# Performance work log

Hardware: AMD Instinct MI355X
Metric: run time of the kernel (lower is better)

Reference implementation:

```python
import jax, jax.numpy as jnp
import numpy as np

C = 256      # channels
G = 8        # groups
K = 9        # 3x3 sampling points (DCNv4 default kernel_size=3)
DWK = 3      # dw_kernel_size (wrapper passes kernel_size=3)
OFFSET_SCALE = 1.0
N, H, W = 8, 64, 64


def setup_inputs() -> dict:
    key = jax.random.key(0)
    ks = jax.random.split(key, 6)
    def init(k, shape, fan):
        return jax.random.normal(k, shape, jnp.float32) * (fan ** -0.5)
    return {
        "x": jax.random.normal(ks[0], (N, C, H, W), jnp.float32),
        "dw_w": init(ks[1], (C, 1, DWK, DWK), DWK * DWK),   # depthwise conv (OIHW, groups=C)
        "dw_b": jnp.zeros((C,), jnp.float32),
        "om_w": init(ks[2], (G * K * 3, C), C) * 0.01,       # offset/mask linear (small offsets)
        "om_b": jnp.zeros((G * K * 3,), jnp.float32),
        "vp_w": init(ks[3], (C, C), C),                      # value_proj
        "vp_b": jnp.zeros((C,), jnp.float32),
        "op_w": init(ks[4], (C, C), C),                      # output_proj (output_bias=False)
    }


def reference(x, dw_w, dw_b, om_w, om_b, vp_w, vp_b, op_w):
    n, c, h, w = x.shape
    cg = c // G
    L = h * w
    # b c h w -> b (h w) c
    xf = x.transpose(0, 2, 3, 1).reshape(n, L, c)
    value = (xf @ vp_w.T + vp_b).reshape(n, L, G, cg)
    # offset/mask branch: depthwise conv on raw input, then linear
    om_in = jax.lax.conv_general_dilated(
        x, dw_w, (1, 1), "SAME", feature_group_count=c,
        dimension_numbers=("NCHW", "OIHW", "NCHW")) + dw_b[None, :, None, None]
    om = om_in.transpose(0, 2, 3, 1).reshape(n, L, c) @ om_w.T + om_b  # (n, L, G*K*3)
    om = om.reshape(n, h, w, G, K * 3)
    off = om[..., : 2 * K].reshape(n, h, w, G, K, 2) * OFFSET_SCALE     # (dy, dx) per point
    mask = om[..., 2 * K:]                                              # (n,h,w,G,K) raw (DCNv4: no softmax)
    # base 3x3 dilation-1 grid centered at each pixel
    d = jnp.arange(-1, 2, dtype=jnp.float32)
    dy, dx = jnp.meshgrid(d, d, indexing="ij")
    base = jnp.stack([dy.ravel(), dx.ravel()], -1)  # (K, 2)
    py = (jnp.arange(h, dtype=jnp.float32).reshape(1, h, 1, 1, 1)
          + base[:, 0].reshape(1, 1, 1, 1, K) + off[..., 0])  # (n,h,w,G,K)
    px = (jnp.arange(w, dtype=jnp.float32).reshape(1, 1, w, 1, 1)
          + base[:, 1].reshape(1, 1, 1, 1, K) + off[..., 1])
    y0 = jnp.floor(py); x0 = jnp.floor(px)
    ty = py - y0; tx = px - x0
    y0i = y0.astype(jnp.int32); x0i = x0.astype(jnp.int32)

    def gather(yi, xi, wgt):
        valid = (yi >= 0) & (yi < h) & (xi >= 0) & (xi < w)
        idx = jnp.clip(yi, 0, h - 1) * w + jnp.clip(xi, 0, w - 1)       # (n,h,w,G,K)
        idx = idx.transpose(0, 1, 2, 4, 3).reshape(n, L * K, G)[..., None]
        g = jnp.take_along_axis(value, idx, axis=1)                     # (n, L*K, G, cg)
        g = g.reshape(n, h, w, K, G, cg).transpose(0, 1, 2, 4, 3, 5)    # (n,h,w,G,K,cg)
        return g * (wgt * valid)[..., None]

    sampled = (gather(y0i,     x0i,     (1 - ty) * (1 - tx))
             + gather(y0i,     x0i + 1, (1 - ty) * tx)
             + gather(y0i + 1, x0i,     ty * (1 - tx))
             + gather(y0i + 1, x0i + 1, ty * tx))
    out = jnp.einsum("nhwgk,nhwgkc->nhwgc", mask, sampled)  # mask-weighted aggregation
    out = out.reshape(n, L, c) @ op_w.T                      # output_proj (no bias)
    # b (h w) c -> b c h w
    return out.reshape(n, h, w, c).transpose(0, 3, 1, 2)
```

## Files before the change

kernel.cpp:

```cpp
#include <hip/hip_runtime.h>
#include <hip/hip_fp16.h>
#include <math.h>

#define N_  8
#define C_  256
#define G_  8
#define CG_ 32
#define K_  9
#define H_  64
#define W_  64
#define L_  (H_*W_)
#define OM_ 216
#define OMP_ 256

using frag_ab = __attribute__((ext_vector_type(8))) short;
using frag_cd = __attribute__((ext_vector_type(4))) float;

__device__ __forceinline__ unsigned short f2bf(float f) {
    unsigned int u = __float_as_uint(f);
    u += 0x7FFFu + ((u >> 16) & 1u);
    return (unsigned short)(u >> 16);
}
__device__ __forceinline__ unsigned short f2h(float f) {
    return __half_as_ushort(__float2half(f));
}

__device__ __forceinline__ void gld16(const void* g, void* l) {
    __builtin_amdgcn_global_load_lds((const __attribute__((address_space(1))) void*)g,
                                     (__attribute__((address_space(3))) void*)l, 16, 0, 0);
}

__device__ __forceinline__ void tapcalc(int l, int k, float offy, float offx, float mk,
                                        float4& wq, uint4& sq) {
    const int y = l >> 6, xp = l & 63;
    float py = (float)(y + k / 3 - 1) + offy;
    float px = (float)(xp + k % 3 - 1) + offx;
    float fy = floorf(py), fx = floorf(px);
    float ty = py - fy, tx = px - fx;
    int y0 = (int)fy, x0i = (int)fx;
    int y1 = y0 + 1, x1 = x0i + 1;
    float vy0 = ((unsigned)y0 < (unsigned)H_) ? 1.f : 0.f;
    float vy1 = ((unsigned)y1 < (unsigned)H_) ? 1.f : 0.f;
    float vx0 = ((unsigned)x0i < (unsigned)W_) ? 1.f : 0.f;
    float vx1 = ((unsigned)x1 < (unsigned)W_) ? 1.f : 0.f;
    int cy0 = min(max(y0, 0), H_ - 1), cy1 = min(max(y1, 0), H_ - 1);
    int cx0 = min(max(x0i, 0), W_ - 1), cx1 = min(max(x1, 0), W_ - 1);
    wq = make_float4(mk * (1.f - ty) * (1.f - tx) * vy0 * vx0,
                     mk * (1.f - ty) * tx         * vy0 * vx1,
                     mk * ty         * (1.f - tx) * vy1 * vx0,
                     mk * ty         * tx         * vy1 * vx1);
    sq = make_uint4((unsigned)((cy0 * W_ + cx0) << 9),
                    (unsigned)((cy0 * W_ + cx1) << 9),
                    (unsigned)((cy1 * W_ + cx0) << 9),
                    (unsigned)((cy1 * W_ + cx1) << 9));
}

__global__ __launch_bounds__(256) void prep_kernel(const float* __restrict__ x,
                                                   const float* __restrict__ w,
                                                   const float* __restrict__ b,
                                                   const float* __restrict__ vp_w,
                                                   const float* __restrict__ om_w,
                                                   const float* __restrict__ om_b,
                                                   const float* __restrict__ op_w,
                                                   unsigned short* __restrict__ xb,
                                                   unsigned short* __restrict__ omb,
                                                   unsigned short* __restrict__ vp_wb,
                                                   unsigned short* __restrict__ om_wb,
                                                   float* __restrict__ om_bp,
                                                   unsigned short* __restrict__ op_wb) {
    const int n = blockIdx.z, y0 = blockIdx.y * 4, c0 = blockIdx.x * 32;
    const int tid = threadIdx.x;
    __shared__ float xs[6][32][66];
    __shared__ __align__(16) unsigned short os[2][64][40];
    for (int i = tid; i < 384; i += 256) {
        int r = i / 64, c = (i / 2) % 32, e = i & 1;
        xs[r][c][e * 65] = 0.f;
    }
    const float* xbase = x + ((size_t)n * C_ + c0) * L_;
    for (int i = tid; i < 6 * 32 * 16; i += 256) {
        int r = i >> 9, rem = i & 511, c = rem >> 4, x4 = (rem & 15) * 4;
        int yy = y0 + r - 1;
        float4 v = make_float4(0.f, 0.f, 0.f, 0.f);
        if ((unsigned)yy < (unsigned)H_) v = *(const float4*)(xbase + (size_t)c * L_ + yy * W_ + x4);
        xs[r][c][1 + x4] = v.x; xs[r][c][2 + x4] = v.y;
        xs[r][c][3 + x4] = v.z; xs[r][c][4 + x4] = v.w;
    }
    __syncthreads();

    const int c = tid & 31, x0 = (tid >> 5) * 8;
    float wv[9];
#pragma unroll
    for (int i = 0; i < 9; i++) wv[i] = w[(c0 + c) * 9 + i];
    const float bias = b[c0 + c];
    const int l = tid >> 2, c8 = (tid & 3) * 8;

    for (int rr = 0; rr < 4; rr++) {
        float o[8];
#pragma unroll
        for (int j = 0; j < 8; j++) o[j] = bias;
#pragma unroll
        for (int r = 0; r < 3; r++) {
            float v[10];
#pragma unroll
            for (int d = 0; d < 10; d++) v[d] = xs[rr + r][c][x0 + d];
#pragma unroll
            for (int j = 0; j < 8; j++)
                o[j] += wv[r * 3] * v[j] + wv[r * 3 + 1] * v[j + 1] + wv[r * 3 + 2] * v[j + 2];
        }
#pragma unroll
        for (int j = 0; j < 8; j++) {
            os[0][x0 + j][c] = f2bf(xs[rr + 1][c][1 + x0 + j]);
            os[1][x0 + j][c] = f2bf(o[j]);
        }
        __syncthreads();
        uint4 va = *(const uint4*)&os[0][l][c8];
        uint4 vc = *(const uint4*)&os[1][l][c8];
        size_t dst = (((size_t)n * 8 + blockIdx.x) * L_ + (y0 + rr) * W_ + l) * 32 + c8;
        *(uint4*)(xb + dst) = va;
        *(uint4*)(omb + dst) = vc;
        __syncthreads();
    }

    if (n == 0) {
        int base = (blockIdx.x + 8 * blockIdx.y) * 256 + tid;
#pragma unroll
        for (int rep2 = 0; rep2 < 2; rep2++) {
            int idx = base + rep2 * 32768;
            vp_wb[idx] = f2bf(vp_w[idx]);
            op_wb[idx] = f2bf(op_w[idx]);
            om_wb[idx] = (idx < OM_ * C_) ? f2bf(om_w[idx]) : (unsigned short)0;
        }
        if (base < OMP_) om_bp[base] = (base < OM_) ? om_b[base] : 0.f;
    }
}

__global__ __launch_bounds__(256, 2) void gemm12_kernel(const unsigned short* __restrict__ xb,
                                                        const unsigned short* __restrict__ omb,
                                                        const unsigned short* __restrict__ vp_wb,
                                                        const unsigned short* __restrict__ om_wb,
                                                        const float* __restrict__ vp_b,
                                                        const float* __restrict__ om_bp,
                                                        unsigned short* __restrict__ valueb,
                                                        float* __restrict__ omf) {
    __shared__ unsigned short As[128 * 32];
    __shared__ unsigned short Bs[256 * 32];
    const int which = blockIdx.z;
    const unsigned short* A = which ? omb : xb;
    const unsigned short* B = which ? om_wb : vp_wb;
    const float* bias = which ? om_bp : vp_b;
    const int tid = threadIdx.x;
    const long i0 = (long)blockIdx.x * 128;
    const int nA = (int)(i0 >> 12);
    const int lofs = (int)(i0 & 4095);
    const int wave = tid >> 6, lane = tid & 63;
    const int iw = (wave & 1) * 64, jw = (wave >> 1) * 128;
    const int lm = lane & 15, kq = lane >> 4;
    const int srow = tid >> 2, scol = (tid & 3) * 8;

    frag_cd acc[4][8];
#pragma unroll
    for (int a = 0; a < 4; a++)
#pragma unroll
        for (int c = 0; c < 8; c++) acc[a][c] = (frag_cd){0.f, 0.f, 0.f, 0.f};

    for (int k0 = 0; k0 < C_; k0 += 32) {
        const unsigned short* ga0 = A + (((size_t)nA * 8 + (k0 >> 5)) * L_ + lofs + srow) * 32 + scol;
        const unsigned short* gb0 = B + (long)srow * C_ + k0 + scol;
        gld16(ga0,             As + tid * 8);
        gld16(ga0 + 64 * 32,   As + 2048 + tid * 8);
        gld16(gb0,             Bs + tid * 8);
        gld16(gb0 + 64 * C_,   Bs + 2048 + tid * 8);
        gld16(gb0 + 128 * C_,  Bs + 4096 + tid * 8);
        gld16(gb0 + 192 * C_,  Bs + 6144 + tid * 8);
        __syncthreads();
        frag_ab af[4], bfr[8];
#pragma unroll
        for (int mi = 0; mi < 4; mi++)
            af[mi] = *(const frag_ab*)&As[(iw + mi * 16 + lm) * 32 + kq * 8];
#pragma unroll
        for (int ni = 0; ni < 8; ni++)
            bfr[ni] = *(const frag_ab*)&Bs[(jw + ni * 16 + lm) * 32 + kq * 8];
#pragma unroll
        for (int mi = 0; mi < 4; mi++)
#pragma unroll
            for (int ni = 0; ni < 8; ni++)
                acc[mi][ni] = __builtin_amdgcn_mfma_f32_16x16x32_bf16(af[mi], bfr[ni], acc[mi][ni], 0, 0, 0);
        __syncthreads();
    }

    float bv[8];
#pragma unroll
    for (int ni = 0; ni < 8; ni++)
        bv[ni] = bias[jw + ni * 16 + lm];

    const long ibase = i0 + iw + kq * 4;
    const int jbase = jw + lm;
#pragma unroll
    for (int mi = 0; mi < 4; mi++) {
#pragma unroll
        for (int ni = 0; ni < 8; ni++) {
            int jj = jbase + ni * 16;
#pragma unroll
            for (int r = 0; r < 4; r++) {
                long i = ibase + mi * 16 + r;
                float v = acc[mi][ni][r] + bv[ni];
                if (which)
                    omf[i * OMP_ + jj] = v;
                else
                    valueb[i * C_ + jj] = f2h(v);
            }
        }
    }
}

__global__ __launch_bounds__(256, 2) void samplegemm_kernel(const unsigned short* __restrict__ value,
                                                            const float* __restrict__ om,
                                                            const unsigned short* __restrict__ opw,
                                                            float* __restrict__ out) {
    const int n = blockIdx.x, l0 = blockIdx.y * 64;
    const int tid = threadIdx.x;
    __shared__ __align__(16) unsigned short interm[64 * 256];
    __shared__ __align__(16) float ombuf[8][224];
    __shared__ float4 wgt[64][9];
    __shared__ uint4  soff[64][9];

    const int wave = tid >> 6, lane = tid & 63;
    const int lp = tid >> 2;
    const int g = lp & 7;
    const int c8i = tid & 3;
    const int slot = tid & 31;
    const char* vbase = (const char*)(value + (size_t)n * L_ * C_);
    const char* vb = vbase + (size_t)(g * CG_ + c8i * 8) * 2;

    const float* omn = om + (size_t)n * L_ * OMP_;
    float* obase = &ombuf[2 * wave][0];

    const int s0row = (lane < 56) ? 0 : 1;
    const int s0idx = (lane < 56) ? lane : (lane - 56);

#define STAGE_OM(REP) { \
        const float* r0_ = omn + (size_t)(l0 + (REP) * 8 + 2 * wave) * OMP_; \
        gld16(r0_ + (size_t)s0row * OMP_ + s0idx * 4, obase); \
        if (lane < 48) gld16(r0_ + OMP_ + (8 + lane) * 4, (char*)obase + 1024); }

    STAGE_OM(0)

    for (int rep = 0; rep < 8; rep++) {
        asm volatile("s_waitcnt vmcnt(0)" ::: "memory");
#pragma unroll
        for (int j = 0; j < 3; j++) {
            if (!(j == 2 && lane >= 16)) {
                int it = lane + j * 64;
                int pl_loc = it / 9, k = it - pl_loc * 9;
                int pl = wave * 16 + pl_loc;
                int pic = pl >> 3;
                const float* ob2 = &ombuf[pic][(pl & 7) * 27];
                float offy = ob2[2 * k], offx = ob2[2 * k + 1], mk = ob2[18 + k];
                float4 wq; uint4 sq;
                tapcalc(l0 + rep * 8 + pic, k, offy, offx, mk, wq, sq);
                wgt[pl][k] = wq; soff[pl][k] = sq;
            }
        }
        asm volatile("" ::: "memory");
        if (rep < 7) STAGE_OM(rep + 1)
        asm volatile("" ::: "memory");
        const int p = rep * 8 + (lp >> 3);
        float acc[8] = {0.f, 0.f, 0.f, 0.f, 0.f, 0.f, 0.f, 0.f};
#pragma unroll
        for (int k = 0; k < K_; k++) {
            float4 wk = wgt[lp][k];
            uint4  ok = soff[lp][k];
            const uint4 v00 = *(const uint4*)(vb + ok.x);
            const uint4 v01 = *(const uint4*)(vb + ok.y);
            const uint4 v10 = *(const uint4*)(vb + ok.z);
            const uint4 v11 = *(const uint4*)(vb + ok.w);
#define ACC8(V, WW) { \
            const __half2* h_ = (const __half2*)&V; \
            acc[0] += WW * __half2float(h_[0].x); acc[1] += WW * __half2float(h_[0].y); \
            acc[2] += WW * __half2float(h_[1].x); acc[3] += WW * __half2float(h_[1].y); \
            acc[4] += WW * __half2float(h_[2].x); acc[5] += WW * __half2float(h_[2].y); \
            acc[6] += WW * __half2float(h_[3].x); acc[7] += WW * __half2float(h_[3].y); }
            ACC8(v00, wk.x) ACC8(v01, wk.y) ACC8(v10, wk.z) ACC8(v11, wk.w)
#undef ACC8
        }
        uint4 pk;
        unsigned short* ps = (unsigned short*)&pk;
#pragma unroll
        for (int i = 0; i < 8; i++) ps[i] = f2bf(acc[i]);
        int phys = slot ^ (p & 7);
        *(uint4*)&interm[p * 256 + phys * 8] = pk;
    }
#undef STAGE_OM
    __syncthreads();

    const int lm = lane & 15, kq = lane >> 4;
    const int q0w = wave * 64;
    frag_cd acc2[4][4];
#pragma unroll
    for (int a = 0; a < 4; a++)
#pragma unroll
        for (int c = 0; c < 4; c++) acc2[a][c] = (frag_cd){0.f, 0.f, 0.f, 0.f};

    for (int k0 = 0; k0 < C_; k0 += 32) {
        frag_ab af[4], bfr[4];
#pragma unroll
        for (int mi = 0; mi < 4; mi++)
            af[mi] = *(const frag_ab*)(opw + (size_t)(q0w + mi * 16 + lm) * C_ + k0 + kq * 8);
#pragma unroll
        for (int ni = 0; ni < 4; ni++) {
            int pxr = ni * 16 + lm;
            int phys = (k0 / 8 + kq) ^ (pxr & 7);
            bfr[ni] = *(const frag_ab*)&interm[pxr * 256 + phys * 8];
        }
#pragma unroll
        for (int mi = 0; mi < 4; mi++)
#pragma unroll
            for (int ni = 0; ni < 4; ni++)
                acc2[mi][ni] = __builtin_amdgcn_mfma_f32_16x16x32_bf16(af[mi], bfr[ni], acc2[mi][ni], 0, 0, 0);
    }

    float* ob = out + (size_t)n * C_ * L_ + l0;
#pragma unroll
    for (int mi = 0; mi < 4; mi++) {
#pragma unroll
        for (int ni = 0; ni < 4; ni++) {
            int pxr = ni * 16 + lm;
#pragma unroll
            for (int r = 0; r < 4; r++) {
                int q = q0w + mi * 16 + kq * 4 + r;
                ob[(size_t)q * L_ + pxr] = acc2[mi][ni][r];
            }
        }
    }
}

extern "C" void kernel_launch(void* const* d_in, const int* in_sizes, int n_in,
                              void* d_out, int out_size, void* d_ws, size_t ws_size,
                              hipStream_t stream) {
    const float* x    = (const float*)d_in[0];
    const float* dw_w = (const float*)d_in[1];
    const float* dw_b = (const float*)d_in[2];
    const float* om_w = (const float*)d_in[3];
    const float* om_b = (const float*)d_in[4];
    const float* vp_w = (const float*)d_in[5];
    const float* vp_b = (const float*)d_in[6];
    const float* op_w = (const float*)d_in[7];
    float* out = (float*)d_out;

    char* ws = (char*)d_ws;
    unsigned short* xb      = (unsigned short*)(ws);
    unsigned short* omb     = (unsigned short*)(ws + 16777216);
    unsigned short* valueb  = (unsigned short*)(ws + 33554432);
    float*          omf     = (float*)(ws + 50331648);
    unsigned short* vp_wb   = (unsigned short*)(ws + 83886080);
    unsigned short* om_wb   = (unsigned short*)(ws + 84017152);
    unsigned short* op_wb   = (unsigned short*)(ws + 84148224);
    float*          om_bp   = (float*)(ws + 84279296);

    prep_kernel<<<dim3(C_ / 32, H_ / 4, N_), 256, 0, stream>>>(
        x, dw_w, dw_b, vp_w, om_w, om_b, op_w,
        xb, omb, vp_wb, om_wb, om_bp, op_wb);
    gemm12_kernel<<<dim3(256, 1, 2), 256, 0, stream>>>(
        xb, omb, vp_wb, om_wb, vp_b, om_bp, valueb, omf);
    samplegemm_kernel<<<dim3(N_, L_ / 64), 256, 0, stream>>>(valueb, omf, op_wb, out);
}
```

Before: 166.8 us.

## Fuse three stages into one cooperative persistent kernel with grid syncs

Merges the prep, gemm12 and samplegemm kernels into a single cooperative launch of 512 blocks, separated by grid-wide syncs, with shared memory reused across stages. Each block handles two prep tiles, one GEMM tile and one sample tile. The aim is to remove kernel launch gaps and tail effects between the three stages. In exchange it adds the cost of grid barriers, and with a 60 KB shared buffer the block count may limit occupancy. It falls back to three separate launches if the cooperative launch fails.

```diff
diff --git a/kernel.cpp b/kernel.cpp
--- a/kernel.cpp
+++ b/kernel.cpp
@@ -1,6 +1,9 @@
 #include <hip/hip_runtime.h>
 #include <hip/hip_fp16.h>
+#include <hip/hip_cooperative_groups.h>
 #include <math.h>
+
+namespace cg = cooperative_groups;
 
 #define N_  8
 #define C_  256
@@ -55,23 +58,19 @@
                     (unsigned)((cy1 * W_ + cx1) << 9));
 }
 
-__global__ __launch_bounds__(256) void prep_kernel(const float* __restrict__ x,
-                                                   const float* __restrict__ w,
-                                                   const float* __restrict__ b,
-                                                   const float* __restrict__ vp_w,
-                                                   const float* __restrict__ om_w,
-                                                   const float* __restrict__ om_b,
-                                                   const float* __restrict__ op_w,
-                                                   unsigned short* __restrict__ xb,
-                                                   unsigned short* __restrict__ omb,
-                                                   unsigned short* __restrict__ vp_wb,
-                                                   unsigned short* __restrict__ om_wb,
-                                                   float* __restrict__ om_bp,
-                                                   unsigned short* __restrict__ op_wb) {
-    const int n = blockIdx.z, y0 = blockIdx.y * 4, c0 = blockIdx.x * 32;
-    const int tid = threadIdx.x;
-    __shared__ float xs[6][32][66];
-    __shared__ __align__(16) unsigned short os[2][64][40];
+
+__device__ __forceinline__ void prep_body(
+    int u, int tid,
+    const float* __restrict__ x, const float* __restrict__ w, const float* __restrict__ b,
+    const float* __restrict__ vp_w, const float* __restrict__ om_w,
+    const float* __restrict__ om_b, const float* __restrict__ op_w,
+    unsigned short* __restrict__ xb, unsigned short* __restrict__ omb,
+    unsigned short* __restrict__ vp_wb, unsigned short* __restrict__ om_wb,
+    float* __restrict__ om_bp, unsigned short* __restrict__ op_wb,
+    float (*xs)[32][66], unsigned short (*os)[64][40])
+{
+    const int bx = u & 7, by = (u >> 3) & 15, n = u >> 7;
+    const int y0 = by * 4, c0 = bx * 32;
     for (int i = tid; i < 384; i += 256) {
         int r = i / 64, c = (i / 2) % 32, e = i & 1;
         xs[r][c][e * 65] = 0.f;
@@ -115,14 +114,14 @@
         __syncthreads();
         uint4 va = *(const uint4*)&os[0][l][c8];
         uint4 vc = *(const uint4*)&os[1][l][c8];
-        size_t dst = (((size_t)n * 8 + blockIdx.x) * L_ + (y0 + rr) * W_ + l) * 32 + c8;
+        size_t dst = (((size_t)n * 8 + bx) * L_ + (y0 + rr) * W_ + l) * 32 + c8;
         *(uint4*)(xb + dst) = va;
         *(uint4*)(omb + dst) = vc;
         __syncthreads();
     }
 
     if (n == 0) {
-        int base = (blockIdx.x + 8 * blockIdx.y) * 256 + tid;
+        int base = (bx + 8 * by) * 256 + tid;
 #pragma unroll
         for (int rep2 = 0; rep2 < 2; rep2++) {
             int idx = base + rep2 * 32768;
@@ -134,22 +133,18 @@
     }
 }
 
-__global__ __launch_bounds__(256, 2) void gemm12_kernel(const unsigned short* __restrict__ xb,
-                                                        const unsigned short* __restrict__ omb,
-                                                        const unsigned short* __restrict__ vp_wb,
-                                                        const unsigned short* __restrict__ om_wb,
-                                                        const float* __restrict__ vp_b,
-                                                        const float* __restrict__ om_bp,
-                                                        unsigned short* __restrict__ valueb,
-                                                        float* __restrict__ omf) {
-    __shared__ unsigned short As[128 * 32];
-    __shared__ unsigned short Bs[256 * 32];
-    const int which = blockIdx.z;
+__device__ __forceinline__ void gemm12_body(
+    int bx, int which, int tid,
+    const unsigned short* __restrict__ xb, const unsigned short* __restrict__ omb,
+    const unsigned short* __restrict__ vp_wb, const unsigned short* __restrict__ om_wb,
+    const float* __restrict__ vp_b, const float* __restrict__ om_bp,
+    unsigned short* __restrict__ valueb, float* __restrict__ omf,
+    unsigned short* As, unsigned short* Bs)
+{
     const unsigned short* A = which ? omb : xb;
     const unsigned short* B = which ? om_wb : vp_wb;
     const float* bias = which ? om_bp : vp_b;
-    const int tid = threadIdx.x;
-    const long i0 = (long)blockIdx.x * 128;
+    const long i0 = (long)bx * 128;
     const int nA = (int)(i0 >> 12);
     const int lofs = (int)(i0 & 4095);
     const int wave = tid >> 6, lane = tid & 63;
@@ -213,17 +208,12 @@
     }
 }
 
-__global__ __launch_bounds__(256, 2) void samplegemm_kernel(const unsigned short* __restrict__ value,
-                                                            const float* __restrict__ om,
-                                                            const unsigned short* __restrict__ opw,
-                                                            float* __restrict__ out) {
-    const int n = blockIdx.x, l0 = blockIdx.y * 64;
-    const int tid = threadIdx.x;
-    __shared__ __align__(16) unsigned short interm[64 * 256];
-    __shared__ __align__(16) float ombuf[8][224];
-    __shared__ float4 wgt[64][9];
-    __shared__ uint4  soff[64][9];
-
+__device__ __forceinline__ void samplegemm_body(
+    int n, int l0, int tid,
+    const unsigned short* __restrict__ value, const float* __restrict__ om,
+    const unsigned short* __restrict__ opw, float* __restrict__ out,
+    unsigned short* interm, float (*ombuf)[224], float4 (*wgt)[9], uint4 (*soff)[9])
+{
     const int wave = tid >> 6, lane = tid & 63;
     const int lp = tid >> 2;
     const int g = lp & 7;
@@ -334,6 +324,91 @@
     }
 }
 
+__global__ __launch_bounds__(256, 2) void fused_kernel(
+    const float* __restrict__ x, const float* __restrict__ dw_w, const float* __restrict__ dw_b,
+    const float* __restrict__ om_w, const float* __restrict__ om_b,
+    const float* __restrict__ vp_w, const float* __restrict__ vp_b,
+    const float* __restrict__ op_w,
+    unsigned short* __restrict__ xb, unsigned short* __restrict__ omb,
+    unsigned short* __restrict__ valueb, float* __restrict__ omf,
+    unsigned short* __restrict__ vp_wb, unsigned short* __restrict__ om_wb,
+    unsigned short* __restrict__ op_wb, float* __restrict__ om_bp,
+    float* __restrict__ out)
+{
+    __shared__ __align__(16) char smem[60928];
+    const int bid = blockIdx.x;
+    const int tid = threadIdx.x;
+    cg::grid_group grid = cg::this_grid();
+
+    {
+        float (*xs)[32][66] = (float(*)[32][66])smem;
+        unsigned short (*os)[64][40] = (unsigned short(*)[64][40])(smem + 50688);
+        prep_body(bid * 2,     tid, x, dw_w, dw_b, vp_w, om_w, om_b, op_w,
+                  xb, omb, vp_wb, om_wb, om_bp, op_wb, xs, os);
+        prep_body(bid * 2 + 1, tid, x, dw_w, dw_b, vp_w, om_w, om_b, op_w,
+                  xb, omb, vp_wb, om_wb, om_bp, op_wb, xs, os);
+    }
+    __threadfence();
+    grid.sync();
+
+    {
+        unsigned short* As = (unsigned short*)smem;
+        unsigned short* Bs = (unsigned short*)(smem + 8192);
+        gemm12_body(bid & 255, bid >> 8, tid, xb, omb, vp_wb, om_wb,
+                    vp_b, om_bp, valueb, omf, As, Bs);
+    }
+    __threadfence();
+    grid.sync();
+
+    {
+        unsigned short* interm = (unsigned short*)smem;
+        float (*ombuf)[224] = (float(*)[224])(smem + 32768);
+        float4 (*wgt)[9]    = (float4(*)[9])(smem + 39936);
+        uint4 (*soff)[9]    = (uint4(*)[9])(smem + 49152);
+        samplegemm_body(bid & 7, (bid >> 3) * 64, tid, valueb, omf, op_wb, out,
+                        interm, ombuf, wgt, soff);
+    }
+}
+
+__global__ __launch_bounds__(256) void prep_kernel(
+    const float* __restrict__ x, const float* __restrict__ w, const float* __restrict__ b,
+    const float* __restrict__ vp_w, const float* __restrict__ om_w,
+    const float* __restrict__ om_b, const float* __restrict__ op_w,
+    unsigned short* __restrict__ xb, unsigned short* __restrict__ omb,
+    unsigned short* __restrict__ vp_wb, unsigned short* __restrict__ om_wb,
+    float* __restrict__ om_bp, unsigned short* __restrict__ op_wb)
+{
+    __shared__ float xs[6][32][66];
+    __shared__ __align__(16) unsigned short os[2][64][40];
+    int u = blockIdx.x + 8 * blockIdx.y + 128 * blockIdx.z;
+    prep_body(u, threadIdx.x, x, w, b, vp_w, om_w, om_b, op_w,
+              xb, omb, vp_wb, om_wb, om_bp, op_wb, xs, os);
+}
+
+__global__ __launch_bounds__(256, 2) void gemm12_kernel(
+    const unsigned short* __restrict__ xb, const unsigned short* __restrict__ omb,
+    const unsigned short* __restrict__ vp_wb, const unsigned short* __restrict__ om_wb,
+    const float* __restrict__ vp_b, const float* __restrict__ om_bp,
+    unsigned short* __restrict__ valueb, float* __restrict__ omf)
+{
+    __shared__ unsigned short As[128 * 32];
+    __shared__ unsigned short Bs[256 * 32];
+    gemm12_body(blockIdx.x, blockIdx.z, threadIdx.x, xb, omb, vp_wb, om_wb,
+                vp_b, om_bp, valueb, omf, As, Bs);
+}
+
+__global__ __launch_bounds__(256, 2) void samplegemm_kernel(
+    const unsigned short* __restrict__ value, const float* __restrict__ om,
+    const unsigned short* __restrict__ opw, float* __restrict__ out)
+{
+    __shared__ __align__(16) unsigned short interm[64 * 256];
+    __shared__ __align__(16) float ombuf[8][224];
+    __shared__ float4 wgt[64][9];
+    __shared__ uint4  soff[64][9];
+    samplegemm_body(blockIdx.x, blockIdx.y * 64, threadIdx.x, value, om, opw, out,
+                    interm, ombuf, wgt, soff);
+}
+
 extern "C" void kernel_launch(void* const* d_in, const int* in_sizes, int n_in,
                               void* d_out, int out_size, void* d_ws, size_t ws_size,
                               hipStream_t stream) {
@@ -357,10 +432,21 @@
     unsigned short* op_wb   = (unsigned short*)(ws + 84148224);
     float*          om_bp   = (float*)(ws + 84279296);
 
-    prep_kernel<<<dim3(C_ / 32, H_ / 4, N_), 256, 0, stream>>>(
-        x, dw_w, dw_b, vp_w, om_w, om_b, op_w,
-        xb, omb, vp_wb, om_wb, om_bp, op_wb);
-    gemm12_kernel<<<dim3(256, 1, 2), 256, 0, stream>>>(
-        xb, omb, vp_wb, om_wb, vp_b, om_bp, valueb, omf);
-    samplegemm_kernel<<<dim3(N_, L_ / 64), 256, 0, stream>>>(valueb, omf, op_wb, out);
-}
+    void* args[] = {
+        (void*)&x, (void*)&dw_w, (void*)&dw_b, (void*)&om_w, (void*)&om_b,
+        (void*)&vp_w, (void*)&vp_b, (void*)&op_w,
+        (void*)&xb, (void*)&omb, (void*)&valueb, (void*)&omf,
+        (void*)&vp_wb, (void*)&om_wb, (void*)&op_wb, (void*)&om_bp,
+        (void*)&out
+    };
+    hipError_t err = hipLaunchCooperativeKernel((void*)fused_kernel,
+                                                dim3(512), dim3(256), args, 0, stream);
+    if (err != hipSuccess) {
+        prep_kernel<<<dim3(C_ / 32, H_ / 4, N_), 256, 0, stream>>>(
+            x, dw_w, dw_b, vp_w, om_w, om_b, op_w,
+            xb, omb, vp_wb, om_wb, om_bp, op_wb);
+        gemm12_kernel<<<dim3(256, 1, 2), 256, 0, stream>>>(
+            xb, omb, vp_wb, om_wb, vp_b, om_bp, valueb, omf);
+        samplegemm_kernel<<<dim3(N_, L_ / 64), 256, 0, stream>>>(valueb, omf, op_wb, out);
+    }
+}
```

Result: slower. 405.0 us (+142.8%).
